# Optimization experiments

Measured on AMD Instinct MI355X. Metric: run time of the kernel, lower is better.

## Reference

```python
import jax, jax.numpy as jnp
import numpy as np

# dims
B, P, H, W = 4, 512, 32, 32
C2 = P // 2            # 256 per-branch channels
HEAD = 4
DH = C2 // HEAD        # 64 head dim
L = H * W              # 1024 tokens
DI = 2 * C2            # 512 mamba d_inner (expand=2)
N = 64                 # d_state
R = (C2 + 15) // 16    # 16 dt_rank
KC = 4                 # d_conv


def setup_inputs() -> dict:
    key = jax.random.key(0)
    ks = jax.random.split(key, 32)
    f32 = jnp.float32
    def nrm(k, shape, s=0.02):
        return jax.random.normal(k, shape, f32) * s
    inp = {}
    inp['x'] = jax.random.normal(ks[0], (B, P, H, W), f32)
    # GambaCell rel-pos + gate conv
    inp['rel_h_c'] = jax.random.normal(ks[1], (1, C2, 1, H), f32)
    inp['rel_w_c'] = jax.random.normal(ks[2], (1, C2, W, 1), f32)
    inp['gate_w'] = nrm(ks[3], (C2, C2, 3))
    inp['gate_b'] = jnp.zeros((C2,), f32)
    # Mamba params
    inp['W_in'] = nrm(ks[4], (2 * DI, C2))
    inp['conv_w'] = nrm(ks[5], (DI, KC), 0.2)
    inp['conv_b'] = jnp.zeros((DI,), f32)
    inp['W_x'] = nrm(ks[6], (R + 2 * N, DI))
    inp['W_dt'] = nrm(ks[7], (DI, R), 0.1)
    inp['b_dt'] = jnp.full((DI,), -4.0, f32)
    inp['A_log'] = jnp.broadcast_to(jnp.log(jnp.arange(1, N + 1, dtype=f32)), (DI, N)).copy()
    inp['D_p'] = jnp.ones((DI,), f32)
    inp['W_out'] = nrm(ks[8], (C2, DI))
    # MHSA params (1x1 convs -> dense)
    inp['Wq'] = nrm(ks[9], (C2, C2)); inp['bq'] = jnp.zeros((C2,), f32)
    inp['Wk'] = nrm(ks[10], (C2, C2)); inp['bk'] = jnp.zeros((C2,), f32)
    inp['Wv'] = nrm(ks[11], (C2, C2)); inp['bv'] = jnp.zeros((C2,), f32)
    inp['rel_h_m'] = jax.random.normal(ks[12], (1, HEAD, DH, 1, H), f32) * 0.02
    inp['rel_w_m'] = jax.random.normal(ks[13], (1, HEAD, DH, W, 1), f32) * 0.02
    inp['reg_qk'] = jax.random.normal(ks[14], (1, L, L), f32)
    inp['reg_v'] = jax.random.normal(ks[15], (1, DH, L), f32)
    # Gating params
    inp['Wa'] = nrm(ks[16], (P, C2)); inp['ba'] = jnp.zeros((P,), f32)
    inp['Wb'] = nrm(ks[17], (P, C2)); inp['bb'] = jnp.zeros((P,), f32)
    inp['Wg'] = nrm(ks[18], (1, P)); inp['bg'] = jnp.zeros((1,), f32)
    return inp


def _silu(t):
    return t * jax.nn.sigmoid(t)


def _conv1x1(w, b, t):  # Conv2d kernel_size=1
    return jnp.einsum('oc,bchw->bohw', w, t) + b[None, :, None, None]


def _mamba(seq, W_in, conv_w, conv_b, W_x, W_dt, b_dt, A_log, D_p, W_out):
    # seq: (B, L, C2)
    Bn = seq.shape[0]
    xz = seq @ W_in.T                       # (B,L,2*DI)
    xi, z = jnp.split(xz, 2, axis=-1)
    # causal depthwise conv1d, kernel 4, left-pad 3, trimmed to L
    xc = jnp.transpose(xi, (0, 2, 1))       # (B,DI,L)
    xp = jnp.pad(xc, ((0, 0), (0, 0), (KC - 1, 0)))
    conv = conv_b[None, :, None]
    for kk in range(KC):
        conv = conv + conv_w[None, :, kk, None] * xp[:, :, kk:kk + L]
    xs = _silu(conv).transpose(0, 2, 1)     # (B,L,DI)
    x_dbl = xs @ W_x.T                      # (B,L,R+2N)
    dt = jax.nn.softplus(x_dbl[..., :R] @ W_dt.T + b_dt)   # (B,L,DI)
    Bm = x_dbl[..., R:R + N]                # (B,L,N)
    Cm = x_dbl[..., R + N:]                 # (B,L,N)
    A = -jnp.exp(A_log)                     # (DI,N)

    def step(h, t):
        dt_t, B_t, C_t, u_t = t             # (B,DI),(B,N),(B,N),(B,DI)
        dA = jnp.exp(dt_t[..., None] * A)   # (B,DI,N)
        h = dA * h + (dt_t * u_t)[..., None] * B_t[:, None, :]
        y = jnp.sum(h * C_t[:, None, :], axis=-1)
        return h, y

    h0 = jnp.zeros((Bn, DI, N), seq.dtype)
    scan_in = (dt.transpose(1, 0, 2), Bm.transpose(1, 0, 2),
               Cm.transpose(1, 0, 2), xs.transpose(1, 0, 2))
    _, ys = jax.lax.scan(step, h0, scan_in)  # (L,B,DI)
    y = ys.transpose(1, 0, 2) + D_p * xs
    y = y * _silu(z)
    return y @ W_out.T                      # (B,L,C2)


def _forward(x, rel_h_c, rel_w_c, gate_w, gate_b, W_in, conv_w, conv_b, W_x,
             W_dt, b_dt, A_log, D_p, W_out, Wq, bq, Wk, bk, Wv, bv,
             rel_h_m, rel_w_m, reg_qk, reg_v, Wa, ba, Wb, bb, Wg, bg):
    Bn = x.shape[0]
    x1, x2 = x[:, :C2], x[:, C2:]
    # --- GambaCell branch ---
    seq = x1.reshape(Bn, C2, L).transpose(0, 2, 1)          # (B,L,C2)
    pos = (rel_h_c + rel_w_c).reshape(1, C2, L).transpose(0, 2, 1)
    seq = seq + pos
    sc = seq.transpose(0, 2, 1)                             # (B,C2,L)
    ctx = jax.nn.sigmoid(
        jax.lax.conv_general_dilated(sc, gate_w, (1,), [(1, 1)],
                                     dimension_numbers=('NCH', 'OIH', 'NCH'))
        + gate_b[None, :, None]).transpose(0, 2, 1)          # (B,L,C2)
    ym = _mamba(seq, W_in, conv_w, conv_b, W_x, W_dt, b_dt, A_log, D_p, W_out)
    # faithful to original: view (B,L,C)->(B,C,H,W) with no permute
    out1 = (ym * ctx).reshape(Bn, C2, H, W)
    # --- MHSA branch ---
    q = _conv1x1(Wq, bq, x2).reshape(Bn, HEAD, DH, L)
    k = _conv1x1(Wk, bk, x2).reshape(Bn, HEAD, DH, L)
    v = _conv1x1(Wv, bv, x2).reshape(Bn, HEAD, DH, L)
    cc = jnp.einsum('bhdi,bhdj->bhij', q, k)                # content-content
    posm = (rel_h_m + rel_w_m).reshape(HEAD, DH, L)
    cp = jnp.einsum('hdi,bhdj->bhij', posm, q)              # position^T @ q
    energy = cc + cp                                         # (B,HEAD,L,L)
    e = jnp.concatenate([energy, jnp.broadcast_to(reg_qk[None], (Bn, 1, L, L))], axis=1)
    vp = jnp.concatenate([v, jnp.broadcast_to(reg_v[None], (Bn, 1, DH, L))], axis=1)
    attn = jax.nn.softmax(e, axis=-1)
    out = jnp.einsum('bndj,bnij->bndi', vp, attn)           # v @ attn^T
    out2 = out[:, :HEAD].reshape(Bn, C2, H, W)
    # --- Gating fusion ---
    a_proj = _conv1x1(Wa, ba, out1)
    b_proj = _conv1x1(Wb, bb, out2)
    ga = jax.nn.sigmoid(_conv1x1(Wg, bg, a_proj))
    gb = jax.nn.sigmoid(_conv1x1(Wg, bg, b_proj))
    return ga * a_proj + gb * b_proj                        # (B,P,H,W)


def reference(x, rel_h_c, rel_w_c, gate_w, gate_b, W_in, conv_w, conv_b, W_x,
              W_dt, b_dt, A_log, D_p, W_out, Wq, bq, Wk, bk, Wv, bv,
              rel_h_m, rel_w_m, reg_qk, reg_v, Wa, ba, Wb, bb, Wg, bg):
    return _forward(x, rel_h_c, rel_w_c, gate_w, gate_b, W_in, conv_w, conv_b,
                    W_x, W_dt, b_dt, A_log, D_p, W_out, Wq, bq, Wk, bk, Wv, bv,
                    rel_h_m, rel_w_m, reg_qk, reg_v, Wa, ba, Wb, bb, Wg, bg)
```

## Files before the change

### kernel.cpp

```cpp
#include <hip/hip_runtime.h>
#include <math.h>

static constexpr int Bn = 4, Pp = 512, C2 = 256, HEAD = 4, DHd = 64;
static constexpr int Ll = 1024, DIi = 512, Nn = 64, Rr = 16, KCc = 4;

#define DEVI __device__ __forceinline__

DEVI float sigf(float x){ return 1.0f/(1.0f+__expf(-x)); }
DEVI float softplusf(float x){ return x > 20.f ? x : log1pf(__expf(x)); }

DEVI unsigned short bfh(float f){
  unsigned int u = __float_as_uint(f);
  return (unsigned short)((u + 0x7FFFu + ((u>>16)&1u)) >> 16);
}
DEVI float bff(unsigned short h){ return __uint_as_float(((unsigned int)h)<<16); }

typedef __attribute__((ext_vector_type(8))) short  bf8v;
typedef __attribute__((ext_vector_type(4))) float  f4v;
typedef __attribute__((ext_vector_type(8))) unsigned short u16x8;

__global__ void k_transpose(const float* __restrict__ x, const float* __restrict__ rh,
                            const float* __restrict__ rw, float* __restrict__ seq,
                            float* __restrict__ x2seq){
  __shared__ float t[32][33];
  int b = blockIdx.z, c0 = blockIdx.y*32, l0 = blockIdx.x*32;
  for (int i = threadIdx.y; i < 32; i += 8)
    t[i][threadIdx.x] = x[((size_t)(b*Pp + c0 + i)*Ll) + l0 + threadIdx.x];
  __syncthreads();
  for (int i = threadIdx.y; i < 32; i += 8){
    int l = l0 + i, c = c0 + threadIdx.x;
    float v = t[threadIdx.x][i];
    if (c < C2){
      float pos = rh[c*32 + (l & 31)] + rw[c*32 + (l >> 5)];
      seq[(size_t)(b*Ll + l)*C2 + c] = v + pos;
    } else {
      x2seq[(size_t)(b*Ll + l)*C2 + (c - C2)] = v;
    }
  }
}

__global__ void __launch_bounds__(256) k_mgemmb(
    const float* __restrict__ A, const float* __restrict__ B,
    float* __restrict__ C, const float* __restrict__ bias,
    int M, int N, int K, int lda, int ldb, int ldc,
    long sA1, long sA2, long sB1, long sB2, long sC1, long sC2, int act)
{
  __shared__ __align__(16) unsigned short Ah[64*40], Al[64*40], Bh[64*40], Bl[64*40];
  int z = blockIdx.z;
  const float* Ab = A + (size_t)((z>>2)*sA1 + (z&3)*sA2);
  const float* Bb = B + (size_t)((z>>2)*sB1 + (z&3)*sB2);
  float*       Cb = C + (size_t)((z>>2)*sC1 + (z&3)*sC2);
  int m0 = blockIdx.y*64, n0 = blockIdx.x*64;
  int t = threadIdx.x;
  int w = t >> 6, l = t & 63;
  int g = l >> 4, r = l & 15;
  int row0 = w*16;

  f4v acc[4];
  #pragma unroll
  for (int j=0;j<4;++j) acc[j] = (f4v){0.f,0.f,0.f,0.f};

  int sr = t >> 2;
  int sc = (t & 3) * 8;

  for (int k0 = 0; k0 < K; k0 += 32){
    {
      const float* src = Ab + (size_t)(m0+sr)*lda + k0 + sc;
      float4 v0 = *(const float4*)(src);
      float4 v1 = *(const float4*)(src+4);
      float f[8] = {v0.x,v0.y,v0.z,v0.w,v1.x,v1.y,v1.z,v1.w};
      u16x8 hv, lv;
      #pragma unroll
      for (int i=0;i<8;++i){
        unsigned short h = bfh(f[i]); hv[i] = h;
        lv[i] = bfh(f[i] - bff(h));
      }
      *(u16x8*)&Ah[sr*40+sc] = hv;
      *(u16x8*)&Al[sr*40+sc] = lv;
    }
    {
      const float* src = Bb + (size_t)(n0+sr)*ldb + k0 + sc;
      float4 v0 = *(const float4*)(src);
      float4 v1 = *(const float4*)(src+4);
      float f[8] = {v0.x,v0.y,v0.z,v0.w,v1.x,v1.y,v1.z,v1.w};
      u16x8 hv, lv;
      #pragma unroll
      for (int i=0;i<8;++i){
        unsigned short h = bfh(f[i]); hv[i] = h;
        lv[i] = bfh(f[i] - bff(h));
      }
      *(u16x8*)&Bh[sr*40+sc] = hv;
      *(u16x8*)&Bl[sr*40+sc] = lv;
    }
    __syncthreads();
    bf8v a_h = *(const bf8v*)&Ah[(row0+r)*40 + g*8];
    bf8v a_l = *(const bf8v*)&Al[(row0+r)*40 + g*8];
    #pragma unroll
    for (int j=0;j<4;++j){
      bf8v b_h = *(const bf8v*)&Bh[(j*16+r)*40 + g*8];
      bf8v b_l = *(const bf8v*)&Bl[(j*16+r)*40 + g*8];
      acc[j] = __builtin_amdgcn_mfma_f32_16x16x32_bf16(a_h, b_h, acc[j], 0, 0, 0);
      acc[j] = __builtin_amdgcn_mfma_f32_16x16x32_bf16(a_h, b_l, acc[j], 0, 0, 0);
      acc[j] = __builtin_amdgcn_mfma_f32_16x16x32_bf16(a_l, b_h, acc[j], 0, 0, 0);
    }
    __syncthreads();
  }
  #pragma unroll
  for (int j=0;j<4;++j){
    int n = n0 + j*16 + r;
    float bv = bias ? bias[n] : 0.f;
    #pragma unroll
    for (int q=0;q<4;++q){
      int m = m0 + row0 + g*4 + q;
      float v = acc[j][q] + bv;
      if (act == 1) v = sigf(v);
      Cb[(size_t)m*ldc + n] = v;
    }
  }
}

__global__ void __launch_bounds__(256) k_gemm(
       const float* __restrict__ A, const float* __restrict__ B,
       float* __restrict__ C, const float* __restrict__ bias,
       int M, int N, int K, int lda, int ldb, int ldc, int act)
{
  __shared__ float As[16][64];
  __shared__ float Bs[16][64];
  int m0 = blockIdx.y*64, n0 = blockIdx.x*64;
  int t = threadIdx.x, tx = t & 15, ty = t >> 4;
  float acc[4][4] = {};
  int arow = t >> 2, akq = (t & 3) * 4;
  for (int k0 = 0; k0 < K; k0 += 16){
    float4 av = *(const float4*)(A + (size_t)(m0+arow)*lda + k0 + akq);
    As[akq+0][arow] = av.x; As[akq+1][arow] = av.y;
    As[akq+2][arow] = av.z; As[akq+3][arow] = av.w;
    float4 bv = make_float4(0.f,0.f,0.f,0.f);
    if (n0 + arow < N) bv = *(const float4*)(B + (size_t)(n0+arow)*ldb + k0 + akq);
    Bs[akq+0][arow]=bv.x; Bs[akq+1][arow]=bv.y;
    Bs[akq+2][arow]=bv.z; Bs[akq+3][arow]=bv.w;
    __syncthreads();
    #pragma unroll
    for (int k = 0; k < 16; ++k){
      float4 a = *(const float4*)&As[k][ty*4];
      float4 b = *(const float4*)&Bs[k][tx*4];
      acc[0][0] = fmaf(a.x,b.x,acc[0][0]); acc[0][1] = fmaf(a.x,b.y,acc[0][1]);
      acc[0][2] = fmaf(a.x,b.z,acc[0][2]); acc[0][3] = fmaf(a.x,b.w,acc[0][3]);
      acc[1][0] = fmaf(a.y,b.x,acc[1][0]); acc[1][1] = fmaf(a.y,b.y,acc[1][1]);
      acc[1][2] = fmaf(a.y,b.z,acc[1][2]); acc[1][3] = fmaf(a.y,b.w,acc[1][3]);
      acc[2][0] = fmaf(a.z,b.x,acc[2][0]); acc[2][1] = fmaf(a.z,b.y,acc[2][1]);
      acc[2][2] = fmaf(a.z,b.z,acc[2][2]); acc[2][3] = fmaf(a.z,b.w,acc[2][3]);
      acc[3][0] = fmaf(a.w,b.x,acc[3][0]); acc[3][1] = fmaf(a.w,b.y,acc[3][1]);
      acc[3][2] = fmaf(a.w,b.z,acc[3][2]); acc[3][3] = fmaf(a.w,b.w,acc[3][3]);
    }
    __syncthreads();
  }
  #pragma unroll
  for (int i = 0; i < 4; ++i){
    int m = m0 + ty*4 + i;
    #pragma unroll
    for (int j = 0; j < 4; ++j){
      int n = n0 + tx*4 + j;
      if (n < N){
        float v = acc[i][j];
        if (bias) v += bias[n];
        if (act == 1) v = sigf(v);
        else if (act == 2) v = softplusf(v);
        C[(size_t)m*ldc + n] = v;
      }
    }
  }
}

__global__ void k_im2col(const float* __restrict__ seq, float* __restrict__ A2){
  int idx = blockIdx.x*256 + threadIdx.x;
  int j  = idx % 768;
  int bl = idx / 768;
  int kk = j >> 8, c = j & 255;
  int l = bl & 1023, b = bl >> 10;
  int ls = l + kk - 1;
  float v = 0.f;
  if (ls >= 0 && ls < Ll) v = seq[(size_t)(b*Ll + ls)*C2 + c];
  A2[idx] = v;
}

__global__ void k_packw(const float* __restrict__ gw, float* __restrict__ W2){
  int idx = blockIdx.x*256 + threadIdx.x;
  int j = idx % 768, o = idx / 768;
  int kk = j >> 8, i = j & 255;
  W2[idx] = gw[(size_t)(o*256 + i)*3 + kk];
}

__global__ void k_dwconv(const float* __restrict__ xz, const float* __restrict__ cw,
                         const float* __restrict__ cb, float* __restrict__ xs){
  int idx = blockIdx.x*256 + threadIdx.x;
  int d = idx & 511; int bl = idx >> 9; int l = bl & 1023; int b = bl >> 10;
  float s = cb[d];
  #pragma unroll
  for (int kk = 0; kk < 4; ++kk){
    int ls = l - 3 + kk;
    if (ls >= 0) s = fmaf(cw[d*4+kk], xz[(size_t)(b*Ll+ls)*1024 + d], s);
  }
  xs[idx] = s * sigf(s);
}

__global__ void __launch_bounds__(64) k_scan3(
    const float* __restrict__ dt, const float* __restrict__ xdbl,
    const float* __restrict__ xs, const float* __restrict__ xz,
    const float* __restrict__ A_log, const float* __restrict__ D_p,
    float* __restrict__ y){
  __shared__ float Bs[32*64];
  __shared__ float Cs[32*64];
  __shared__ float pb[32*65];
  __shared__ float sdt[32], sdtu[32];
  int lane = threadIdx.x;
  int wid  = blockIdx.x;
  int b = wid >> 9, d = wid & 511;
  float Ac = -__expf(A_log[d*64 + lane]);
  float Dp = D_p[d];
  float h = 0.f;
  size_t base = (size_t)b*Ll;
  int jl = lane & 31;
  bool lo = lane < 32;
  for (int c0 = 0; c0 < Ll; c0 += 32){
    size_t rowj = base + c0 + jl;
    float uv = 0.f, zv = 0.f;
    if (lo){
      float dtv = dt[rowj*512 + d];
      uv = xs[rowj*512 + d];
      zv = xz[rowj*1024 + 512 + d];
      sdt[jl]  = dtv;
      sdtu[jl] = dtv*uv;
    }
    for (int l = 0; l < 32; ++l){
      size_t r2 = (base + c0 + l)*144;
      Bs[l*64 + lane] = xdbl[r2 + 16 + lane];
      Cs[l*64 + lane] = xdbl[r2 + 80 + lane];
    }
    __syncthreads();
    #pragma unroll
    for (int l = 0; l < 32; ++l){
      float dA = __expf(sdt[l]*Ac);
      h = fmaf(dA, h, sdtu[l]*Bs[l*64 + lane]);
      pb[l*65 + lane] = h*Cs[l*64 + lane];
    }
    __syncthreads();
    {
      const float* rp = &pb[jl*65 + (lo ? 0 : 32)];
      float s0=0.f, s1=0.f, s2=0.f, s3=0.f;
      #pragma unroll
      for (int n = 0; n < 32; n += 4){
        s0 += rp[n]; s1 += rp[n+1]; s2 += rp[n+2]; s3 += rp[n+3];
      }
      float p = (s0+s1)+(s2+s3);
      p += __shfl_xor(p, 32);
      if (lo) y[rowj*512 + d] = (p + Dp*uv) * (zv * sigf(zv));
    }
    __syncthreads();
  }
}

__global__ void k_pack_ab(const float* __restrict__ qt, const float* __restrict__ kt,
                          const float* __restrict__ rhm, const float* __restrict__ rwm,
                          float* __restrict__ Ab, float* __restrict__ Bb){
  int idx = blockIdx.x*256 + threadIdx.x;
  int dd = idx & 127;
  int i  = (idx >> 7) & 1023;
  int h  = (idx >> 17) & 3;
  int b  = idx >> 19;
  float av, bv;
  if (dd < 64){
    size_t q = (size_t)(b*Ll + i)*C2 + h*64 + dd;
    av = qt[q]; bv = kt[q];
  } else {
    int d = dd - 64;
    av = rhm[(h*64+d)*32 + (i & 31)] + rwm[(h*64+d)*32 + (i >> 5)];
    bv = qt[(size_t)(b*Ll + i)*C2 + h*64 + d];
  }
  Ab[idx] = av; Bb[idx] = bv;
}

__global__ void k_vtrans(const float* __restrict__ vt, float* __restrict__ vT){
  __shared__ float t[32][33];
  int b = blockIdx.z, c0 = blockIdx.y*32, j0 = blockIdx.x*32;
  for (int i = threadIdx.y; i < 32; i += 8)
    t[i][threadIdx.x] = vt[(size_t)(b*Ll + j0 + i)*C2 + c0 + threadIdx.x];
  __syncthreads();
  for (int i = threadIdx.y; i < 32; i += 8)
    vT[((size_t)(b*C2 + c0 + i))*Ll + j0 + threadIdx.x] = t[threadIdx.x][i];
}

__global__ void __launch_bounds__(256) k_softmax(float* __restrict__ e){
  __shared__ float red[4];
  __shared__ float red2[4];
  size_t row = blockIdx.x;
  float* p = e + row*1024;
  int t = threadIdx.x;
  float v0 = p[t], v1 = p[t+256], v2 = p[t+512], v3 = p[t+768];
  float mx = fmaxf(fmaxf(v0,v1), fmaxf(v2,v3));
  #pragma unroll
  for (int off=32; off; off>>=1) mx = fmaxf(mx, __shfl_xor(mx, off));
  if ((t&63)==0) red[t>>6] = mx;
  __syncthreads();
  mx = fmaxf(fmaxf(red[0],red[1]), fmaxf(red[2],red[3]));
  v0 = __expf(v0-mx); v1 = __expf(v1-mx); v2 = __expf(v2-mx); v3 = __expf(v3-mx);
  float s = v0+v1+v2+v3;
  #pragma unroll
  for (int off=32; off; off>>=1) s += __shfl_xor(s, off);
  if ((t&63)==0) red2[t>>6] = s;
  __syncthreads();
  s = red2[0]+red2[1]+red2[2]+red2[3];
  float inv = 1.0f/s;
  p[t] = v0*inv; p[t+256] = v1*inv; p[t+512] = v2*inv; p[t+768] = v3*inv;
}

__global__ void k_mulshuf(const float* __restrict__ ym, const float* __restrict__ ctx,
                          float* __restrict__ out1t){
  __shared__ float t[32][33];
  int b = blockIdx.z >> 2, s1 = blockIdx.z & 3;
  int c0 = blockIdx.y*32, s00 = blockIdx.x*32;
  for (int i = threadIdx.y; i < 32; i += 8){
    int c = c0 + i;
    int l = c*4 + s1;
    size_t off = ((size_t)(b*Ll + l))*C2 + s00 + threadIdx.x;
    t[i][threadIdx.x] = ym[off] * ctx[off];
  }
  __syncthreads();
  for (int i = threadIdx.y; i < 32; i += 8){
    int s0 = s00 + i, c = c0 + threadIdx.x;
    int s = s1*256 + s0;
    out1t[((size_t)(b*Ll + s))*C2 + c] = t[threadIdx.x][i];
  }
}

__global__ void __launch_bounds__(256) k_gates(
    const float* __restrict__ ap, const float* __restrict__ bp,
    const float* __restrict__ Wg, const float* __restrict__ bg, float* __restrict__ g){
  __shared__ float ra[4], rb[4];
  int bl = blockIdx.x; int t = threadIdx.x;
  float sa = 0.f, sb = 0.f;
  const float* a = ap + (size_t)bl*512;
  const float* bq = bp + (size_t)bl*512;
  for (int pp = t; pp < 512; pp += 256){ float w = Wg[pp]; sa = fmaf(w, a[pp], sa); sb = fmaf(w, bq[pp], sb); }
  #pragma unroll
  for (int off=32; off; off>>=1){ sa += __shfl_xor(sa,off); sb += __shfl_xor(sb,off); }
  if ((t&63)==0){ ra[t>>6]=sa; rb[t>>6]=sb; }
  __syncthreads();
  if (t==0){
    float b0 = bg[0];
    g[bl]        = sigf(ra[0]+ra[1]+ra[2]+ra[3] + b0);
    g[4096 + bl] = sigf(rb[0]+rb[1]+rb[2]+rb[3] + b0);
  }
}

__global__ void k_final(const float* __restrict__ ap, const float* __restrict__ bp,
                        const float* __restrict__ g, float* __restrict__ out){
  int bpid = blockIdx.x; int b = bpid >> 9, p = bpid & 511;
  for (int l = threadIdx.x; l < Ll; l += 256){
    int bl = b*Ll + l;
    float ga = g[bl], gb = g[4096 + bl];
    out[((size_t)(b*Pp + p) << 10) + l] =
        ga*ap[(size_t)bl*512 + p] + gb*bp[(size_t)bl*512 + p];
  }
}

static inline void mgemm(hipStream_t s, const float* A, const float* B, float* C,
                         const float* bias, int M, int N, int K, int lda, int ldb, int ldc,
                         int act){
  dim3 g(N/64, M/64, 1), blk(256);
  k_mgemmb<<<g, blk, 0, s>>>(A,B,C,bias,M,N,K,lda,ldb,ldc, 0,0,0,0,0,0, act);
}

extern "C" void kernel_launch(void* const* d_in, const int* in_sizes, int n_in,
                              void* d_out, int out_size, void* d_ws, size_t ws_size,
                              hipStream_t stream) {
  const float* x      = (const float*)d_in[0];
  const float* rh_c   = (const float*)d_in[1];
  const float* rw_c   = (const float*)d_in[2];
  const float* gate_w = (const float*)d_in[3];
  const float* gate_b = (const float*)d_in[4];
  const float* W_in   = (const float*)d_in[5];
  const float* conv_w = (const float*)d_in[6];
  const float* conv_b = (const float*)d_in[7];
  const float* W_x    = (const float*)d_in[8];
  const float* W_dt   = (const float*)d_in[9];
  const float* b_dt   = (const float*)d_in[10];
  const float* A_log  = (const float*)d_in[11];
  const float* D_p    = (const float*)d_in[12];
  const float* W_out  = (const float*)d_in[13];
  const float* Wq     = (const float*)d_in[14];
  const float* bq     = (const float*)d_in[15];
  const float* Wk     = (const float*)d_in[16];
  const float* bk     = (const float*)d_in[17];
  const float* Wv     = (const float*)d_in[18];
  const float* bv     = (const float*)d_in[19];
  const float* rhm    = (const float*)d_in[20];
  const float* rwm    = (const float*)d_in[21];
  const float* Wa     = (const float*)d_in[24];
  const float* ba     = (const float*)d_in[25];
  const float* Wb     = (const float*)d_in[26];
  const float* bb     = (const float*)d_in[27];
  const float* Wg     = (const float*)d_in[28];
  const float* bg     = (const float*)d_in[29];
  float* out = (float*)d_out;
  float* ws  = (float*)d_ws;

  float* seq    = ws;
  float* x2seq  = ws +  1048576;
  float* qt     = ws +  2097152;
  float* kt     = ws +  3145728;
  float* vt     = ws +  4194304;
  float* Abuf   = ws +  5242880;
  float* Bbuf   = ws +  7340032;
  float* arena  = ws +  9437184;
  float* out2   = ws + 26214400;
  float* out1   = ws + 27262976;
  float* aproj  = ws + 28311552;
  float* bproj  = ws + 30408704;
  float* gates  = ws + 32505856;
  float* W2     = ws + 32514048;
  float* A2   = arena;
  float* ctx  = arena +  3145728;
  float* xz   = arena +  4194304;
  float* xs   = arena +  8388608;
  float* xdbl = arena + 10485760;
  float* dtb  = arena + 11075584;
  float* yb   = arena + 13172736;
  float* ym   = arena + 15269888;
  float* energy = arena;
  float* vT   = aproj;

  k_transpose<<<dim3(32,16,4), dim3(32,8), 0, stream>>>(x, rh_c, rw_c, seq, x2seq);

  mgemm(stream, x2seq, Wq, qt, bq, 4096,256,256, 256,256,256, 0);
  mgemm(stream, x2seq, Wk, kt, bk, 4096,256,256, 256,256,256, 0);
  mgemm(stream, x2seq, Wv, vt, bv, 4096,256,256, 256,256,256, 0);
  k_pack_ab<<<8192, 256, 0, stream>>>(qt, kt, rhm, rwm, Abuf, Bbuf);
  k_vtrans<<<dim3(32,8,4), dim3(32,8), 0, stream>>>(vt, vT);
  {
    dim3 g(16, 16, 16), blk(256);
    k_mgemmb<<<g, blk, 0, stream>>>(Abuf, Bbuf, energy, nullptr,
        1024,1024,128, 128,128,1024,
        4L*131072, 131072, 4L*131072, 131072, 4L*1048576, 1048576, 0);
  }
  k_softmax<<<16384, 256, 0, stream>>>(energy);
  {
    dim3 g(1, 16, 16), blk(256);
    k_mgemmb<<<g, blk, 0, stream>>>(energy, vT, out2, nullptr,
        1024,64,1024, 1024,1024,256,
        4L*1048576, 1048576, 262144, 65536, 262144, 64, 0);
  }

  k_packw<<<768, 256, 0, stream>>>(gate_w, W2);
  k_im2col<<<12288, 256, 0, stream>>>(seq, A2);
  mgemm(stream, A2, W2, ctx, gate_b, 4096,256,768, 768,768,256, 1);
  mgemm(stream, seq, W_in, xz, nullptr, 4096,1024,256, 256,256,1024, 0);
  k_dwconv<<<8192, 256, 0, stream>>>(xz, conv_w, conv_b, xs);
  {
    dim3 g(3, 64, 1), blk(256);
    k_gemm<<<g, blk, 0, stream>>>(xs, W_x, xdbl, nullptr, 4096,144,512, 512,512,144, 0);
  }
  {
    dim3 g(8, 64, 1), blk(256);
    k_gemm<<<g, blk, 0, stream>>>(xdbl, W_dt, dtb, b_dt, 4096,512,16, 144,16,512, 2);
  }
  k_scan3<<<2048, 64, 0, stream>>>(dtb, xdbl, xs, xz, A_log, D_p, yb);
  mgemm(stream, yb, W_out, ym, nullptr, 4096,256,512, 512,512,256, 0);
  k_mulshuf<<<dim3(8,8,16), dim3(32,8), 0, stream>>>(ym, ctx, out1);

  mgemm(stream, out1, Wa, aproj, ba, 4096,512,256, 256,256,512, 0);
  mgemm(stream, out2, Wb, bproj, bb, 4096,512,256, 256,256,512, 0);
  k_gates<<<4096, 256, 0, stream>>>(aproj, bproj, Wg, bg, gates);
  k_final<<<2048, 256, 0, stream>>>(aproj, bproj, gates, out);
}
```

Before: 606.2 us.

## Transpose scan inputs/outputs to channel-major to coalesce selective-scan memory access

Replaces the dt GEMM with a kernel that computes softplus(dt) and dt*u and writes them in (b,d,l) layout. The scan can then read contiguous per-channel sequences and broadcast them with shuffles instead of shared memory, and it writes a transposed y. A separate transpose kernel applies the D skip and SiLU(z) gate. This removes the strided 512-stride loads in the serial scan, at the cost of two extra launches and extra transposed buffers that reuse the Abuf/Bbuf workspace.

```diff
diff --git a/kernel.cpp b/kernel.cpp
--- a/kernel.cpp
+++ b/kernel.cpp
@@ -203,33 +203,53 @@
   xs[idx] = s * sigf(s);
 }
 
-__global__ void __launch_bounds__(64) k_scan3(
-    const float* __restrict__ dt, const float* __restrict__ xdbl,
-    const float* __restrict__ xs, const float* __restrict__ xz,
-    const float* __restrict__ A_log, const float* __restrict__ D_p,
-    float* __restrict__ y){
+__global__ void k_pret(const float* __restrict__ xdbl, const float* __restrict__ xs,
+                       const float* __restrict__ W_dt, const float* __restrict__ b_dt,
+                       float* __restrict__ dtT, float* __restrict__ dtuT){
+  __shared__ float X[32][17];
+  __shared__ float Wd[32][17];
+  __shared__ float xsb[32][33];
+  int b = blockIdx.z, d0 = blockIdx.y*32, l0 = blockIdx.x*32;
+  int tx = threadIdx.x, ty = threadIdx.y;
+  for (int i = ty; i < 32; i += 8){
+    if (tx < 16)      X[i][tx]      = xdbl[(size_t)(b*Ll + l0 + i)*144 + tx];
+    else              Wd[i][tx-16]  = W_dt[(size_t)(d0 + i)*16 + tx - 16];
+    xsb[i][tx] = xs[(size_t)(b*Ll + l0 + i)*512 + d0 + tx];
+  }
+  __syncthreads();
+  for (int dy = ty; dy < 32; dy += 8){
+    int d = d0 + dy;
+    float v = b_dt[d];
+    #pragma unroll
+    for (int r = 0; r < 16; ++r) v = fmaf(Wd[dy][r], X[tx][r], v);
+    float dt = softplusf(v);
+    size_t o = ((size_t)(b*512 + d))*Ll + l0 + tx;
+    dtT[o]  = dt;
+    dtuT[o] = dt * xsb[tx][dy];
+  }
+}
+
+__global__ void __launch_bounds__(64) k_scan4(
+    const float* __restrict__ dtT, const float* __restrict__ dtuT,
+    const float* __restrict__ xdbl, const float* __restrict__ A_log,
+    float* __restrict__ yT){
   __shared__ float Bs[32*64];
   __shared__ float Cs[32*64];
   __shared__ float pb[32*65];
-  __shared__ float sdt[32], sdtu[32];
   int lane = threadIdx.x;
   int wid  = blockIdx.x;
   int b = wid >> 9, d = wid & 511;
   float Ac = -__expf(A_log[d*64 + lane]);
-  float Dp = D_p[d];
   float h = 0.f;
   size_t base = (size_t)b*Ll;
+  size_t bd   = (size_t)wid*Ll;
   int jl = lane & 31;
   bool lo = lane < 32;
   for (int c0 = 0; c0 < Ll; c0 += 32){
-    size_t rowj = base + c0 + jl;
-    float uv = 0.f, zv = 0.f;
+    float dtv = 0.f, duv = 0.f;
     if (lo){
-      float dtv = dt[rowj*512 + d];
-      uv = xs[rowj*512 + d];
-      zv = xz[rowj*1024 + 512 + d];
-      sdt[jl]  = dtv;
-      sdtu[jl] = dtv*uv;
+      dtv = dtT[bd + c0 + lane];
+      duv = dtuT[bd + c0 + lane];
     }
     for (int l = 0; l < 32; ++l){
       size_t r2 = (base + c0 + l)*144;
@@ -239,8 +259,10 @@
     __syncthreads();
     #pragma unroll
     for (int l = 0; l < 32; ++l){
-      float dA = __expf(sdt[l]*Ac);
-      h = fmaf(dA, h, sdtu[l]*Bs[l*64 + lane]);
+      float sdt = __shfl(dtv, l);
+      float sdu = __shfl(duv, l);
+      float dA = __expf(sdt*Ac);
+      h = fmaf(dA, h, sdu*Bs[l*64 + lane]);
       pb[l*65 + lane] = h*Cs[l*64 + lane];
     }
     __syncthreads();
@@ -253,9 +275,28 @@
       }
       float p = (s0+s1)+(s2+s3);
       p += __shfl_xor(p, 32);
-      if (lo) y[rowj*512 + d] = (p + Dp*uv) * (zv * sigf(zv));
-    }
-    __syncthreads();
+      if (lo) yT[bd + c0 + jl] = p;
+    }
+    __syncthreads();
+  }
+}
+
+__global__ void k_ytrans(const float* __restrict__ yT, const float* __restrict__ xs,
+                         const float* __restrict__ xz, const float* __restrict__ D_p,
+                         float* __restrict__ y){
+  __shared__ float t[32][33];
+  int b = blockIdx.z, d0 = blockIdx.y*32, l0 = blockIdx.x*32;
+  int tx = threadIdx.x, ty = threadIdx.y;
+  for (int i = ty; i < 32; i += 8)
+    t[i][tx] = yT[((size_t)(b*512 + d0 + i))*Ll + l0 + tx];
+  __syncthreads();
+  for (int i = ty; i < 32; i += 8){
+    int d = d0 + tx;
+    size_t bl = (size_t)b*Ll + l0 + i;
+    float p  = t[tx][i];
+    float u  = xs[bl*512 + d];
+    float zv = xz[bl*1024 + 512 + d];
+    y[bl*512 + d] = (p + D_p[d]*u) * (zv * sigf(zv));
   }
 }
 
@@ -423,11 +464,13 @@
   float* xz   = arena +  4194304;
   float* xs   = arena +  8388608;
   float* xdbl = arena + 10485760;
-  float* dtb  = arena + 11075584;
+  float* yT   = arena + 11075584;
   float* yb   = arena + 13172736;
   float* ym   = arena + 15269888;
   float* energy = arena;
   float* vT   = aproj;
+  float* dtT  = Abuf;
+  float* dtuT = Bbuf;
 
   k_transpose<<<dim3(32,16,4), dim3(32,8), 0, stream>>>(x, rh_c, rw_c, seq, x2seq);
 
@@ -459,11 +502,9 @@
     dim3 g(3, 64, 1), blk(256);
     k_gemm<<<g, blk, 0, stream>>>(xs, W_x, xdbl, nullptr, 4096,144,512, 512,512,144, 0);
   }
-  {
-    dim3 g(8, 64, 1), blk(256);
-    k_gemm<<<g, blk, 0, stream>>>(xdbl, W_dt, dtb, b_dt, 4096,512,16, 144,16,512, 2);
-  }
-  k_scan3<<<2048, 64, 0, stream>>>(dtb, xdbl, xs, xz, A_log, D_p, yb);
+  k_pret<<<dim3(32,16,4), dim3(32,8), 0, stream>>>(xdbl, xs, W_dt, b_dt, dtT, dtuT);
+  k_scan4<<<2048, 64, 0, stream>>>(dtT, dtuT, xdbl, A_log, yT);
+  k_ytrans<<<dim3(32,16,4), dim3(32,8), 0, stream>>>(yT, xs, xz, D_p, yb);
   mgemm(stream, yb, W_out, ym, nullptr, 4096,256,512, 512,512,256, 0);
   k_mulshuf<<<dim3(8,8,16), dim3(32,8), 0, stream>>>(ym, ctx, out1);
 
```

Result: slower. 645.2 us (+6.4%).
